# Optimization experiments

Hardware: AMD Instinct MI355X
Metric: run time of the kernel (lower is better)

The kernel has to match this reference:

```python
import jax, jax.numpy as jnp
import numpy as np

B, N_ROWS, N_COLS, CTRL = 16384, 2048, 128, 1024
EPS = 1e-16


def setup_inputs() -> dict:
    key = jax.random.key(0)
    k1, k2, k3 = jax.random.split(key, 3)
    x = jax.random.normal(k1, (B, CTRL), dtype=jnp.float32)
    W_fc = jax.random.normal(k2, (CTRL, N_COLS + 6), dtype=jnp.float32) * 0.02
    b_fc = jnp.zeros((N_COLS + 6,), dtype=jnp.float32)
    M = jax.random.normal(k3, (N_ROWS, N_COLS), dtype=jnp.float32)
    # initial weighting: softmax of bias with w_bias[0]=100 -> ~one-hot at row 0
    w_bias = jnp.zeros((N_ROWS,), dtype=jnp.float32).at[0].set(100.0)
    w_prev = jnp.broadcast_to(jax.nn.softmax(w_bias), (B, N_ROWS))
    return {"x": x, "W_fc": W_fc, "b_fc": b_fc, "M": M, "w_prev": w_prev}


def reference(x, W_fc, b_fc, M, w_prev):
    # dense projection + split
    h = x @ W_fc + b_fc                      # [B, N_COLS+6]
    k = h[:, :N_COLS]                        # [B, N_COLS]
    beta = jax.nn.softplus(h[:, N_COLS:N_COLS + 1])          # [B, 1]
    g = jax.nn.sigmoid(h[:, N_COLS + 1:N_COLS + 2])          # [B, 1]
    s = jax.nn.softmax(h[:, N_COLS + 2:N_COLS + 5], axis=-1) # [B, 3]
    gamma = 1.0 + jax.nn.softplus(h[:, N_COLS + 5:N_COLS + 6])  # [B, 1]

    # content addressing: cosine similarity against every memory row
    k_norm = jnp.linalg.norm(k, axis=-1, keepdims=True)       # [B, 1]
    M_norm = jnp.linalg.norm(M, axis=-1)                      # [N_ROWS]
    sim = (k @ M.T) / (k_norm * M_norm[None, :] + EPS)        # [B, N_ROWS]
    w_c = jax.nn.softmax(beta * sim, axis=-1)

    # interpolation gate
    w_g = g * w_c + (1.0 - g) * w_prev

    # circular shift convolution (shifts -1, 0, +1)
    w_tilde = (s[:, 0:1] * jnp.roll(w_g, 1, axis=1)
               + s[:, 1:2] * w_g
               + s[:, 2:3] * jnp.roll(w_g, -1, axis=1))

    # sharpening
    w_pow = (w_tilde + EPS) ** gamma
    w = w_pow / jnp.sum(w_pow, axis=-1, keepdims=True)

    # weighted read
    r = w @ M                                                 # [B, N_COLS]
    return r
```

## Files before the change

### kernel.cpp

```cpp
#include <hip/hip_runtime.h>
#include <hip/hip_bf16.h>

#define NB     16384
#define NR     2048
#define NC     128
#define KCTRL  1024
#define EPSF   1e-16f
#define ESTR   2056
#define R1ROWS 32

typedef __attribute__((ext_vector_type(8))) short bf16x8;
typedef __attribute__((ext_vector_type(4))) float f32x4;

__device__ __forceinline__ float softplus_f(float x) {
    return fmaxf(x, 0.f) + log1pf(__expf(-fabsf(x)));
}
__device__ __forceinline__ unsigned short f2bf(float f) {
    __hip_bfloat16 h = __float2bfloat16(f);
    return *(unsigned short*)&h;
}
__device__ __forceinline__ float bf2f(unsigned short u) {
    __hip_bfloat16 h;
    *(unsigned short*)&h = u;
    return __bfloat162float(h);
}

__device__ __forceinline__ size_t swz(int n, int k, int nch) {
    return ((size_t)((n >> 4) * nch + (k >> 5)) * 64 + ((k >> 3) & 3) * 16 + (n & 15)) * 8 + (k & 7);
}

__global__ __launch_bounds__(64) void prep_all(const float* __restrict__ M,
                                               unsigned short* __restrict__ Mb_sw,
                                               unsigned short* __restrict__ Mt_sw,
                                               float* __restrict__ imn,
                                               const float* __restrict__ W,
                                               unsigned short* __restrict__ Wt_sw) {
    const int bid = blockIdx.x;
    const int l = threadIdx.x;
    if (bid < NR) {
        const int i = bid;
        const float v0 = M[(size_t)i * NC + l];
        const float v1 = M[(size_t)i * NC + 64 + l];
        Mb_sw[swz(i, l, 4)]      = f2bf(v0);
        Mb_sw[swz(i, 64 + l, 4)] = f2bf(v1);
        Mt_sw[swz(l, i, 64)]      = f2bf(v0);
        Mt_sw[swz(64 + l, i, 64)] = f2bf(v1);
        float s = v0 * v0 + v1 * v1;
        #pragma unroll
        for (int m = 1; m < 64; m <<= 1) s += __shfl_xor(s, m);
        if (l == 0) imn[i] = 1.f / sqrtf(s);
    } else {
        const int k = bid - NR;
        Wt_sw[swz(l, k, 32)]      = f2bf(W[(size_t)k * 134 + l]);
        Wt_sw[swz(64 + l, k, 32)] = f2bf(W[(size_t)k * 134 + 64 + l]);
        if (l < 6) {
            Wt_sw[swz(128 + l, k, 32)] = f2bf(W[(size_t)k * 134 + 128 + l]);
        }
    }
}

__global__ __launch_bounds__(512) void fc_gemm(const float* __restrict__ x,
                                               const unsigned short* __restrict__ Wt_sw,
                                               const float* __restrict__ bfc,
                                               unsigned short* __restrict__ kb,
                                               float* __restrict__ scal_g) {
    __shared__ __align__(16) unsigned short x_s[R1ROWS][136];
    __shared__ float ksum[R1ROWS];
    __shared__ float h6s[R1ROWS][6];

    const int tid  = threadIdx.x;
    const int w    = tid >> 6;
    const int lane = tid & 63;
    const int quad = lane >> 4;
    const int l16  = lane & 15;
    const int rg   = w >> 2;
    const int cq   = w & 3;
    const int b0   = blockIdx.x * R1ROWS;

    if (tid < R1ROWS) ksum[tid] = 0.f;

    f32x4 accA = {0.f, 0.f, 0.f, 0.f};
    f32x4 accB = {0.f, 0.f, 0.f, 0.f};
    f32x4 accH = {0.f, 0.f, 0.f, 0.f};
    const unsigned short* wb = Wt_sw + lane * 8;
    const size_t tA = (size_t)(cq * 2) * 32;
    const size_t tB = (size_t)(cq * 2 + 1) * 32;
    const size_t tH = (size_t)8 * 32;

    for (int kc = 0; kc < 8; kc++) {
        #pragma unroll
        for (int p = 0; p < 2; p++) {
            const int idx = p * 512 + tid;
            const int row = idx >> 5;
            const int c4  = idx & 31;
            const float4 v = *(const float4*)(x + (size_t)(b0 + row) * KCTRL + kc * 128 + c4 * 4);
            unsigned short* d = &x_s[row][c4 * 4];
            d[0] = f2bf(v.x); d[1] = f2bf(v.y); d[2] = f2bf(v.z); d[3] = f2bf(v.w);
        }
        __syncthreads();
        #pragma unroll
        for (int ks = 0; ks < 4; ks++) {
            const int sg = kc * 4 + ks;
            const bf16x8 a  = *(const bf16x8*)&x_s[rg * 16 + l16][ks * 32 + quad * 8];
            const bf16x8 bA = *(const bf16x8*)(wb + (tA + sg) * 512);
            const bf16x8 bB = *(const bf16x8*)(wb + (tB + sg) * 512);
            accA = __builtin_amdgcn_mfma_f32_16x16x32_bf16(a, bA, accA, 0, 0, 0);
            accB = __builtin_amdgcn_mfma_f32_16x16x32_bf16(a, bB, accB, 0, 0, 0);
            if (cq == 0) {
                const bf16x8 bH = *(const bf16x8*)(wb + (tH + sg) * 512);
                accH = __builtin_amdgcn_mfma_f32_16x16x32_bf16(a, bH, accH, 0, 0, 0);
            }
        }
        __syncthreads();
    }

    float part[4];
    #pragma unroll
    for (int reg = 0; reg < 4; reg++) {
        const int m = quad * 4 + reg;
        const size_t grow = (size_t)(b0 + rg * 16 + m);
        const float vA = accA[reg] + bfc[cq * 32 + l16];
        const float vB = accB[reg] + bfc[cq * 32 + 16 + l16];
        kb[grow * NC + cq * 32 + l16]      = f2bf(vA);
        kb[grow * NC + cq * 32 + 16 + l16] = f2bf(vB);
        part[reg] = vA * vA + vB * vB;
    }
    #pragma unroll
    for (int s = 1; s < 16; s <<= 1) {
        #pragma unroll
        for (int reg = 0; reg < 4; reg++) part[reg] += __shfl_xor(part[reg], s);
    }
    if (l16 == 0) {
        #pragma unroll
        for (int reg = 0; reg < 4; reg++)
            atomicAdd(&ksum[rg * 16 + quad * 4 + reg], part[reg]);
    }
    if (cq == 0 && l16 < 6) {
        #pragma unroll
        for (int reg = 0; reg < 4; reg++)
            h6s[rg * 16 + quad * 4 + reg][l16] = accH[reg] + bfc[128 + l16];
    }
    __syncthreads();

    if (tid < R1ROWS) {
        const float kn = sqrtf(ksum[tid]);
        const float* h = h6s[tid];
        const float beta = softplus_f(h[0]);
        const float g = 1.f / (1.f + __expf(-h[1]));
        const float m3 = fmaxf(h[2], fmaxf(h[3], h[4]));
        const float e0 = __expf(h[2] - m3), e1 = __expf(h[3] - m3), e2 = __expf(h[4] - m3);
        const float inv = 1.f / (e0 + e1 + e2);
        float* sgp = scal_g + (size_t)(b0 + tid) * 6;
        sgp[0] = beta / kn;
        sgp[1] = g;
        sgp[2] = e0 * inv;
        sgp[3] = e1 * inv;
        sgp[4] = e2 * inv;
        sgp[5] = 1.f + softplus_f(h[5]);
    }
}

__global__ __launch_bounds__(512, 4) void head_ntm(const unsigned short* __restrict__ kb,
                                                   const float* __restrict__ scal_g,
                                                   const unsigned short* __restrict__ Mb_sw,
                                                   const unsigned short* __restrict__ Mt_sw,
                                                   const float* __restrict__ imn,
                                                   const float* __restrict__ wprev,
                                                   float* __restrict__ out) {
    __shared__ __align__(16) unsigned short E_s[16][ESTR];
    __shared__ float scal_s[16][6];
    __shared__ float wred[16][8];
    __shared__ float fa_s[16], fc_s[16], invZ_s[16];

    const int tid  = threadIdx.x;
    const int w    = tid >> 6;
    const int lane = tid & 63;
    const int quad = lane >> 4;
    const int l16  = lane & 15;
    const int b0   = blockIdx.x * 16;

    if (tid < 16) {
        const float* sgp = scal_g + (size_t)(b0 + tid) * 6;
        #pragma unroll
        for (int j = 0; j < 6; j++) scal_s[tid][j] = sgp[j];
    }
    __syncthreads();

    {
        float cbs[4];
        #pragma unroll
        for (int reg = 0; reg < 4; reg++) cbs[reg] = scal_s[quad * 4 + reg][0];

        const unsigned short* kbp = kb + (size_t)(b0 + l16) * NC + quad * 8;
        const bf16x8 af0 = *(const bf16x8*)(kbp);
        const bf16x8 af1 = *(const bf16x8*)(kbp + 32);
        const bf16x8 af2 = *(const bf16x8*)(kbp + 64);
        const bf16x8 af3 = *(const bf16x8*)(kbp + 96);

        const unsigned short* bpw = Mb_sw + (size_t)(w * 16) * 2048 + lane * 8;
        bf16x8 f00 = *(const bf16x8*)(bpw);
        bf16x8 f01 = *(const bf16x8*)(bpw + 512);
        bf16x8 f02 = *(const bf16x8*)(bpw + 1024);
        bf16x8 f03 = *(const bf16x8*)(bpw + 1536);
        bf16x8 f10 = *(const bf16x8*)(bpw + 2048);
        bf16x8 f11 = *(const bf16x8*)(bpw + 2048 + 512);
        bf16x8 f12 = *(const bf16x8*)(bpw + 2048 + 1024);
        bf16x8 f13 = *(const bf16x8*)(bpw + 2048 + 1536);
        float im0 = imn[(w * 16 + 0) * 16 + l16];
        float im1 = imn[(w * 16 + 1) * 16 + l16];

        float Sp[4] = {0.f, 0.f, 0.f, 0.f};
        #pragma unroll
        for (int t = 0; t < 16; t += 2) {
            {
                const int nt = w * 16 + t;
                f32x4 aA = {0.f, 0.f, 0.f, 0.f};
                f32x4 aB = {0.f, 0.f, 0.f, 0.f};
                aA = __builtin_amdgcn_mfma_f32_16x16x32_bf16(af0, f00, aA, 0, 0, 0);
                aB = __builtin_amdgcn_mfma_f32_16x16x32_bf16(af2, f02, aB, 0, 0, 0);
                aA = __builtin_amdgcn_mfma_f32_16x16x32_bf16(af1, f01, aA, 0, 0, 0);
                aB = __builtin_amdgcn_mfma_f32_16x16x32_bf16(af3, f03, aB, 0, 0, 0);
                const float imc = im0;
                if (t < 14) {
                    const unsigned short* bp = Mb_sw + (size_t)(nt + 2) * 2048 + lane * 8;
                    f00 = *(const bf16x8*)(bp);
                    f01 = *(const bf16x8*)(bp + 512);
                    f02 = *(const bf16x8*)(bp + 1024);
                    f03 = *(const bf16x8*)(bp + 1536);
                    im0 = imn[(nt + 2) * 16 + l16];
                }
                const int n0 = nt * 16;
                #pragma unroll
                for (int reg = 0; reg < 4; reg++) {
                    const float e = __expf((aA[reg] + aB[reg]) * cbs[reg] * imc);
                    E_s[quad * 4 + reg][n0 + l16] = f2bf(e);
                    Sp[reg] += e;
                }
            }
            {
                const int nt = w * 16 + t + 1;
                f32x4 aA = {0.f, 0.f, 0.f, 0.f};
                f32x4 aB = {0.f, 0.f, 0.f, 0.f};
                aA = __builtin_amdgcn_mfma_f32_16x16x32_bf16(af0, f10, aA, 0, 0, 0);
                aB = __builtin_amdgcn_mfma_f32_16x16x32_bf16(af2, f12, aB, 0, 0, 0);
                aA = __builtin_amdgcn_mfma_f32_16x16x32_bf16(af1, f11, aA, 0, 0, 0);
                aB = __builtin_amdgcn_mfma_f32_16x16x32_bf16(af3, f13, aB, 0, 0, 0);
                const float imc = im1;
                if (t < 13) {
                    const unsigned short* bp = Mb_sw + (size_t)(nt + 2) * 2048 + lane * 8;
                    f10 = *(const bf16x8*)(bp);
                    f11 = *(const bf16x8*)(bp + 512);
                    f12 = *(const bf16x8*)(bp + 1024);
                    f13 = *(const bf16x8*)(bp + 1536);
                    im1 = imn[(nt + 2) * 16 + l16];
                }
                const int n0 = nt * 16;
                #pragma unroll
                for (int reg = 0; reg < 4; reg++) {
                    const float e = __expf((aA[reg] + aB[reg]) * cbs[reg] * imc);
                    E_s[quad * 4 + reg][n0 + l16] = f2bf(e);
                    Sp[reg] += e;
                }
            }
        }
        #pragma unroll
        for (int s = 1; s < 16; s <<= 1) {
            #pragma unroll
            for (int reg = 0; reg < 4; reg++) Sp[reg] += __shfl_xor(Sp[reg], s);
        }
        if (l16 == 0) {
            #pragma unroll
            for (int reg = 0; reg < 4; reg++) wred[quad * 4 + reg][w] = Sp[reg];
        }
    }
    __syncthreads();
    if (tid < 16) {
        float S = 0.f;
        #pragma unroll
        for (int i = 0; i < 8; i++) S += wred[tid][i];
        const float g = scal_s[tid][1];
        fa_s[tid] = g / S;
        fc_s[tid] = 1.f - g;
    }
    __syncthreads();

    {
        const int row  = tid >> 5;
        const int g    = tid & 31;
        const int base = tid & 32;
        const float s0 = scal_s[row][2], s1 = scal_s[row][3], s2 = scal_s[row][4];
        const float gmm = scal_s[row][5];
        const float fa = fa_s[row], fcm = fc_s[row];
        const float* wp = wprev + (size_t)(b0 + row) * NR;

        int c0 = g * 8;
        bf16x8 E8c = *(const bf16x8*)&E_s[row][c0];
        float eLc  = bf2f(E_s[row][(c0 + NR - 1) & (NR - 1)]);
        float eRc  = bf2f(E_s[row][c0 + 8]);
        float4 wac = *(const float4*)(wp + c0);
        float4 wbc = *(const float4*)(wp + c0 + 4);
        float wpLc = wp[(c0 + NR - 1) & (NR - 1)];
        float wpRc = wp[c0 + 8];

        float Zp = 0.f, carry = 0.f, E0sav = 0.f;
        #pragma unroll
        for (int j = 0; j < 8; j++) {
            bf16x8 E8n; float eLn = 0.f, eRn = 0.f, wpLn = 0.f, wpRn = 0.f;
            float4 wan, wbn;
            if (j < 7) {
                const int c1 = c0 + 256;
                E8n  = *(const bf16x8*)&E_s[row][c1];
                eLn  = bf2f(E_s[row][c1 - 1]);
                eRn  = bf2f(E_s[row][(c1 + 8) & (NR - 1)]);
                wan  = *(const float4*)(wp + c1);
                wbn  = *(const float4*)(wp + c1 + 4);
                wpLn = wp[c1 - 1];
                wpRn = wp[(c1 + 8) & (NR - 1)];
            }
            float ef[8];
            #pragma unroll
            for (int i = 0; i < 8; i++) ef[i] = bf2f((unsigned short)E8c[i]);
            if (j == 0) E0sav = __shfl(ef[0], base);
            const float eL = (g == 0 && j > 0) ? carry : eLc;
            const float eR = (g == 31 && j == 7) ? E0sav : eRc;
            carry = __shfl(ef[7], base + 31);

            float wg[10];
            wg[0] = fmaf(fa, eL,    fcm * wpLc);
            wg[1] = fmaf(fa, ef[0], fcm * wac.x);
            wg[2] = fmaf(fa, ef[1], fcm * wac.y);
            wg[3] = fmaf(fa, ef[2], fcm * wac.z);
            wg[4] = fmaf(fa, ef[3], fcm * wac.w);
            wg[5] = fmaf(fa, ef[4], fcm * wbc.x);
            wg[6] = fmaf(fa, ef[5], fcm * wbc.y);
            wg[7] = fmaf(fa, ef[6], fcm * wbc.z);
            wg[8] = fmaf(fa, ef[7], fcm * wbc.w);
            wg[9] = fmaf(fa, eR,    fcm * wpRc);

            bf16x8 out8;
            #pragma unroll
            for (int i = 0; i < 8; i++) {
                const float wt = fmaf(s0, wg[i], fmaf(s1, wg[i + 1], s2 * wg[i + 2])) + EPSF;
                const float pw = exp2f(gmm * log2f(wt));
                Zp += pw;
                out8[i] = (short)f2bf(pw);
            }
            *(bf16x8*)&E_s[row][c0] = out8;

            c0 += 256;
            E8c = E8n; eLc = eLn; eRc = eRn;
            wac = wan; wbc = wbn; wpLc = wpLn; wpRc = wpRn;
        }
        #pragma unroll
        for (int s = 1; s < 32; s <<= 1) Zp += __shfl_xor(Zp, s);
        if (g == 0) invZ_s[row] = 1.f / Zp;
    }
    __syncthreads();

    {
        f32x4 acc0 = {0.f, 0.f, 0.f, 0.f};
        f32x4 acc1 = {0.f, 0.f, 0.f, 0.f};
        f32x4 acc2 = {0.f, 0.f, 0.f, 0.f};
        f32x4 acc3 = {0.f, 0.f, 0.f, 0.f};
        const unsigned short* bp = Mt_sw + (size_t)w * 32768 + lane * 8;
        bf16x8 c00 = *(const bf16x8*)(bp);
        bf16x8 c01 = *(const bf16x8*)(bp + 512);
        bf16x8 c02 = *(const bf16x8*)(bp + 1024);
        bf16x8 c03 = *(const bf16x8*)(bp + 1536);
        bf16x8 c10 = *(const bf16x8*)(bp + 2048);
        bf16x8 c11 = *(const bf16x8*)(bp + 2048 + 512);
        bf16x8 c12 = *(const bf16x8*)(bp + 2048 + 1024);
        bf16x8 c13 = *(const bf16x8*)(bp + 2048 + 1536);

        #pragma unroll
        for (int k0 = 0; k0 < NR; k0 += 256) {
            {
                const bf16x8 a0 = *(const bf16x8*)&E_s[l16][k0 + quad * 8];
                const bf16x8 a1 = *(const bf16x8*)&E_s[l16][k0 + 32 + quad * 8];
                const bf16x8 a2 = *(const bf16x8*)&E_s[l16][k0 + 64 + quad * 8];
                const bf16x8 a3 = *(const bf16x8*)&E_s[l16][k0 + 96 + quad * 8];
                acc0 = __builtin_amdgcn_mfma_f32_16x16x32_bf16(a0, c00, acc0, 0, 0, 0);
                acc1 = __builtin_amdgcn_mfma_f32_16x16x32_bf16(a1, c01, acc1, 0, 0, 0);
                acc2 = __builtin_amdgcn_mfma_f32_16x16x32_bf16(a2, c02, acc2, 0, 0, 0);
                acc3 = __builtin_amdgcn_mfma_f32_16x16x32_bf16(a3, c03, acc3, 0, 0, 0);
                if (k0 < NR - 256) {
                    const unsigned short* np = bp + (size_t)((k0 >> 5) + 8) * 512;
                    c00 = *(const bf16x8*)(np);
                    c01 = *(const bf16x8*)(np + 512);
                    c02 = *(const bf16x8*)(np + 1024);
                    c03 = *(const bf16x8*)(np + 1536);
                }
            }
            {
                const int k1 = k0 + 128;
                const bf16x8 a0 = *(const bf16x8*)&E_s[l16][k1 + quad * 8];
                const bf16x8 a1 = *(const bf16x8*)&E_s[l16][k1 + 32 + quad * 8];
                const bf16x8 a2 = *(const bf16x8*)&E_s[l16][k1 + 64 + quad * 8];
                const bf16x8 a3 = *(const bf16x8*)&E_s[l16][k1 + 96 + quad * 8];
                acc0 = __builtin_amdgcn_mfma_f32_16x16x32_bf16(a0, c10, acc0, 0, 0, 0);
                acc1 = __builtin_amdgcn_mfma_f32_16x16x32_bf16(a1, c11, acc1, 0, 0, 0);
                acc2 = __builtin_amdgcn_mfma_f32_16x16x32_bf16(a2, c12, acc2, 0, 0, 0);
                acc3 = __builtin_amdgcn_mfma_f32_16x16x32_bf16(a3, c13, acc3, 0, 0, 0);
                if (k0 < NR - 384) {
                    const unsigned short* np = bp + (size_t)((k0 >> 5) + 12) * 512;
                    c10 = *(const bf16x8*)(np);
                    c11 = *(const bf16x8*)(np + 512);
                    c12 = *(const bf16x8*)(np + 1024);
                    c13 = *(const bf16x8*)(np + 1536);
                }
            }
        }
        #pragma unroll
        for (int reg = 0; reg < 4; reg++) {
            const int m = quad * 4 + reg;
            const float v = (acc0[reg] + acc1[reg]) + (acc2[reg] + acc3[reg]);
            out[(size_t)(b0 + m) * NC + w * 16 + l16] = v * invZ_s[m];
        }
    }
}

extern "C" void kernel_launch(void* const* d_in, const int* in_sizes, int n_in,
                              void* d_out, int out_size, void* d_ws, size_t ws_size,
                              hipStream_t stream) {
    const float* x     = (const float*)d_in[0];
    const float* Wfc   = (const float*)d_in[1];
    const float* bfc   = (const float*)d_in[2];
    const float* M     = (const float*)d_in[3];
    const float* wprev = (const float*)d_in[4];
    float* out = (float*)d_out;

    char* ws = (char*)d_ws;
    float*          imn    = (float*)(ws);
    unsigned short* Mb_sw  = (unsigned short*)(ws + 8192);
    unsigned short* Mt_sw  = (unsigned short*)(ws + 532480);
    unsigned short* Wt_sw  = (unsigned short*)(ws + 1056768);
    unsigned short* kb     = (unsigned short*)(ws + 1351680);
    float*          scal_g = (float*)(ws + 5545984);

    hipLaunchKernelGGL(prep_all, dim3(NR + KCTRL), dim3(64), 0, stream,
                       M, Mb_sw, Mt_sw, imn, Wfc, Wt_sw);
    hipLaunchKernelGGL(fc_gemm, dim3(NB / R1ROWS), dim3(512), 0, stream,
                       x, Wt_sw, bfc, kb, scal_g);
    hipLaunchKernelGGL(head_ntm, dim3(NB / 16), dim3(512), 0, stream,
                       kb, scal_g, Mb_sw, Mt_sw, imn, wprev, out);
}
```

Baseline: 304.8 us.

## Double rows per fc_gemm block, register-prefetch x chunks, widen per-wave N tile

```diff
diff --git a/kernel.cpp b/kernel.cpp
--- a/kernel.cpp
+++ b/kernel.cpp
@@ -7,7 +7,7 @@
 #define KCTRL  1024
 #define EPSF   1e-16f
 #define ESTR   2056
-#define R1ROWS 32
+#define R1ROWS 64
 
 typedef __attribute__((ext_vector_type(8))) short bf16x8;
 typedef __attribute__((ext_vector_type(4))) float f32x4;
@@ -65,7 +65,7 @@
                                                unsigned short* __restrict__ kb,
                                                float* __restrict__ scal_g) {
     __shared__ __align__(16) unsigned short x_s[R1ROWS][136];
-    __shared__ float ksum[R1ROWS];
+    __shared__ float wred[R1ROWS][2];
     __shared__ float h6s[R1ROWS][6];
 
     const int tid  = threadIdx.x;
@@ -73,57 +73,80 @@
     const int lane = tid & 63;
     const int quad = lane >> 4;
     const int l16  = lane & 15;
-    const int rg   = w >> 2;
-    const int cq   = w & 3;
+    const int rg   = w >> 1;
+    const int half = w & 1;
+    const int tb   = half * 4;
     const int b0   = blockIdx.x * R1ROWS;
 
-    if (tid < R1ROWS) ksum[tid] = 0.f;
-
-    f32x4 accA = {0.f, 0.f, 0.f, 0.f};
-    f32x4 accB = {0.f, 0.f, 0.f, 0.f};
+    f32x4 acc0 = {0.f, 0.f, 0.f, 0.f};
+    f32x4 acc1 = {0.f, 0.f, 0.f, 0.f};
+    f32x4 acc2 = {0.f, 0.f, 0.f, 0.f};
+    f32x4 acc3 = {0.f, 0.f, 0.f, 0.f};
     f32x4 accH = {0.f, 0.f, 0.f, 0.f};
     const unsigned short* wb = Wt_sw + lane * 8;
-    const size_t tA = (size_t)(cq * 2) * 32;
-    const size_t tB = (size_t)(cq * 2 + 1) * 32;
-    const size_t tH = (size_t)8 * 32;
+
+    float4 st0, st1, st2, st3;
+    {
+        const int r0 = tid >> 5, c4 = (tid & 31) * 4;
+        const float* xp = x + (size_t)(b0 + r0) * KCTRL + c4;
+        st0 = *(const float4*)(xp);
+        st1 = *(const float4*)(xp + 16 * KCTRL);
+        st2 = *(const float4*)(xp + 32 * KCTRL);
+        st3 = *(const float4*)(xp + 48 * KCTRL);
+    }
 
     for (int kc = 0; kc < 8; kc++) {
-        #pragma unroll
-        for (int p = 0; p < 2; p++) {
-            const int idx = p * 512 + tid;
-            const int row = idx >> 5;
-            const int c4  = idx & 31;
-            const float4 v = *(const float4*)(x + (size_t)(b0 + row) * KCTRL + kc * 128 + c4 * 4);
-            unsigned short* d = &x_s[row][c4 * 4];
-            d[0] = f2bf(v.x); d[1] = f2bf(v.y); d[2] = f2bf(v.z); d[3] = f2bf(v.w);
+        {
+            const int r0 = tid >> 5, c4 = (tid & 31) * 4;
+            unsigned short* d0 = &x_s[r0][c4];
+            d0[0] = f2bf(st0.x); d0[1] = f2bf(st0.y); d0[2] = f2bf(st0.z); d0[3] = f2bf(st0.w);
+            unsigned short* d1 = &x_s[r0 + 16][c4];
+            d1[0] = f2bf(st1.x); d1[1] = f2bf(st1.y); d1[2] = f2bf(st1.z); d1[3] = f2bf(st1.w);
+            unsigned short* d2 = &x_s[r0 + 32][c4];
+            d2[0] = f2bf(st2.x); d2[1] = f2bf(st2.y); d2[2] = f2bf(st2.z); d2[3] = f2bf(st2.w);
+            unsigned short* d3 = &x_s[r0 + 48][c4];
+            d3[0] = f2bf(st3.x); d3[1] = f2bf(st3.y); d3[2] = f2bf(st3.z); d3[3] = f2bf(st3.w);
         }
         __syncthreads();
+        if (kc < 7) {
+            const int r0 = tid >> 5, c4 = (tid & 31) * 4;
+            const float* xp = x + (size_t)(b0 + r0) * KCTRL + (kc + 1) * 128 + c4;
+            st0 = *(const float4*)(xp);
+            st1 = *(const float4*)(xp + 16 * KCTRL);
+            st2 = *(const float4*)(xp + 32 * KCTRL);
+            st3 = *(const float4*)(xp + 48 * KCTRL);
+        }
         #pragma unroll
         for (int ks = 0; ks < 4; ks++) {
             const int sg = kc * 4 + ks;
             const bf16x8 a  = *(const bf16x8*)&x_s[rg * 16 + l16][ks * 32 + quad * 8];
-            const bf16x8 bA = *(const bf16x8*)(wb + (tA + sg) * 512);
-            const bf16x8 bB = *(const bf16x8*)(wb + (tB + sg) * 512);
-            accA = __builtin_amdgcn_mfma_f32_16x16x32_bf16(a, bA, accA, 0, 0, 0);
-            accB = __builtin_amdgcn_mfma_f32_16x16x32_bf16(a, bB, accB, 0, 0, 0);
-            if (cq == 0) {
-                const bf16x8 bH = *(const bf16x8*)(wb + (tH + sg) * 512);
+            const bf16x8 b0v = *(const bf16x8*)(wb + (size_t)((tb + 0) * 32 + sg) * 512);
+            const bf16x8 b1v = *(const bf16x8*)(wb + (size_t)((tb + 1) * 32 + sg) * 512);
+            const bf16x8 b2v = *(const bf16x8*)(wb + (size_t)((tb + 2) * 32 + sg) * 512);
+            const bf16x8 b3v = *(const bf16x8*)(wb + (size_t)((tb + 3) * 32 + sg) * 512);
+            acc0 = __builtin_amdgcn_mfma_f32_16x16x32_bf16(a, b0v, acc0, 0, 0, 0);
+            acc1 = __builtin_amdgcn_mfma_f32_16x16x32_bf16(a, b1v, acc1, 0, 0, 0);
+            acc2 = __builtin_amdgcn_mfma_f32_16x16x32_bf16(a, b2v, acc2, 0, 0, 0);
+            acc3 = __builtin_amdgcn_mfma_f32_16x16x32_bf16(a, b3v, acc3, 0, 0, 0);
+            if (half == 0) {
+                const bf16x8 bH = *(const bf16x8*)(wb + (size_t)(8 * 32 + sg) * 512);
                 accH = __builtin_amdgcn_mfma_f32_16x16x32_bf16(a, bH, accH, 0, 0, 0);
             }
         }
         __syncthreads();
     }
 
-    float part[4];
+    float part[4] = {0.f, 0.f, 0.f, 0.f};
     #pragma unroll
-    for (int reg = 0; reg < 4; reg++) {
-        const int m = quad * 4 + reg;
-        const size_t grow = (size_t)(b0 + rg * 16 + m);
-        const float vA = accA[reg] + bfc[cq * 32 + l16];
-        const float vB = accB[reg] + bfc[cq * 32 + 16 + l16];
-        kb[grow * NC + cq * 32 + l16]      = f2bf(vA);
-        kb[grow * NC + cq * 32 + 16 + l16] = f2bf(vB);
-        part[reg] = vA * vA + vB * vB;
+    for (int t = 0; t < 4; t++) {
+        const f32x4 ac = (t == 0) ? acc0 : (t == 1) ? acc1 : (t == 2) ? acc2 : acc3;
+        const float bb = bfc[(tb + t) * 16 + l16];
+        #pragma unroll
+        for (int reg = 0; reg < 4; reg++) {
+            const float v = ac[reg] + bb;
+            kb[(size_t)(b0 + rg * 16 + quad * 4 + reg) * NC + (tb + t) * 16 + l16] = f2bf(v);
+            part[reg] += v * v;
+        }
     }
     #pragma unroll
     for (int s = 1; s < 16; s <<= 1) {
@@ -133,17 +156,18 @@
     if (l16 == 0) {
         #pragma unroll
         for (int reg = 0; reg < 4; reg++)
-            atomicAdd(&ksum[rg * 16 + quad * 4 + reg], part[reg]);
-    }
-    if (cq == 0 && l16 < 6) {
+            wred[rg * 16 + quad * 4 + reg][half] = part[reg];
+    }
+    if (half == 0 && l16 < 6) {
+        const float bh = bfc[128 + l16];
         #pragma unroll
         for (int reg = 0; reg < 4; reg++)
-            h6s[rg * 16 + quad * 4 + reg][l16] = accH[reg] + bfc[128 + l16];
+            h6s[rg * 16 + quad * 4 + reg][l16] = accH[reg] + bh;
     }
     __syncthreads();
 
     if (tid < R1ROWS) {
-        const float kn = sqrtf(ksum[tid]);
+        const float kn = sqrtf(wred[tid][0] + wred[tid][1]);
         const float* h = h6s[tid];
         const float beta = softplus_f(h[0]);
         const float g = 1.f / (1.f + __expf(-h[1]));
```

Result: no change. 307.8 us (+1.0%).
